# Kernel optimization log

Hardware: AMD Instinct MI355X
Metric: run time of the kernel (lower is better)

## Reference

```python
import jax, jax.numpy as jnp
import numpy as np

N_NODES = 100000
N_EDGES = 1600000
N_FEAT = 128
HIDDEN = 64
N_CLASSES = 40


def setup_inputs() -> dict:
    key = jax.random.key(0)
    ks = jax.random.split(key, 4)
    x = jax.random.normal(ks[0], (N_NODES, N_FEAT), dtype=jnp.float32)
    edge_index = jax.random.randint(ks[1], (2, N_EDGES), 0, N_NODES, dtype=jnp.int64)
    # Glorot-style init like PyG GCNConv
    W1 = jax.random.normal(ks[2], (N_FEAT, HIDDEN), dtype=jnp.float32) * (1.0 / np.sqrt(N_FEAT))
    b1 = jnp.zeros((HIDDEN,), dtype=jnp.float32)
    W2 = jax.random.normal(ks[3], (HIDDEN, N_CLASSES), dtype=jnp.float32) * (1.0 / np.sqrt(HIDDEN))
    b2 = jnp.zeros((N_CLASSES,), dtype=jnp.float32)
    return {"x": x, "edge_index": edge_index, "W1": W1, "b1": b1, "W2": W2, "b2": b2}


def _gcn_conv(x, src, dst, norm, W, b, n_nodes):
    # PyG GCNConv: transform first, then normalized scatter-add aggregation
    h = x @ W                                   # [N, out]
    msg = h[src] * norm[:, None]                # [E+N, out] gather
    out = jax.ops.segment_sum(msg, dst, num_segments=n_nodes)  # scatter-add
    return out + b


def _norm_and_loops(edge_index, n_nodes):
    # add self-loops, symmetric normalization deg^{-1/2} A_hat deg^{-1/2}
    loop = jnp.arange(n_nodes, dtype=edge_index.dtype)
    src = jnp.concatenate([edge_index[0], loop])
    dst = jnp.concatenate([edge_index[1], loop])
    deg = jax.ops.segment_sum(jnp.ones_like(dst, dtype=jnp.float32), dst, num_segments=n_nodes)
    dinv = jnp.where(deg > 0, jax.lax.rsqrt(jnp.maximum(deg, 1.0)), 0.0)
    norm = dinv[src] * dinv[dst]
    return src, dst, norm


def reference(x, edge_index, W1, b1, W2, b2):
    n_nodes = x.shape[0]
    src, dst, norm = _norm_and_loops(edge_index, n_nodes)
    h = _gcn_conv(x, src, dst, norm, W1, b1, n_nodes)
    h = jax.nn.relu(h)
    h = _gcn_conv(h, src, dst, norm, W2, b2, n_nodes)
    return jax.nn.log_softmax(h, axis=1)
```

## Files before the change

kernel.cpp:

```cpp
#include <hip/hip_runtime.h>
#include <hip/hip_bf16.h>
#include <string.h>

#define N_FEAT 128
#define HIDDEN 64
#define N_CLS  40
#define FILL_BLOCKS 2048
#define CHUNK_EDGES 16384
#define STAGE_CAP 4096
#define B_BITS 6
#define SRC_BITS 17

typedef __bf16 bf16x8 __attribute__((ext_vector_type(8)));
typedef float  f32x4  __attribute__((ext_vector_type(4)));

union Frag { unsigned u[4]; bf16x8 v; };

static __device__ inline int get_xcc() {
    return (int)(__builtin_amdgcn_s_getreg((3 << 11) | 20) & 7u);
}


static __device__ inline unsigned pack_bf16(float a, float b) {
    unsigned ba = __float_as_uint(a);
    unsigned bb = __float_as_uint(b);
    unsigned ra = (ba + 0x7fffu + ((ba >> 16) & 1u)) >> 16;
    unsigned rb = (bb + 0x7fffu + ((bb >> 16) & 1u)) >> 16;
    return (ra & 0xffffu) | (rb << 16);
}

static __device__ inline float2 unpack_bf16(unsigned v) {
    return make_float2(__uint_as_float(v << 16), __uint_as_float(v & 0xffff0000u));
}


__global__ void detect_layout_kernel(const int* __restrict__ ei, int* __restrict__ flag) {
    int lane = threadIdx.x;
    int v = ei[2 * lane + 1];
    unsigned long long b = __ballot(v != 0);
    if (lane == 0) flag[0] = (b == 0ull) ? 1 : 0;
}


__global__ __launch_bounds__(256) void bucket_hist_kernel(const int* __restrict__ ei,
                                                          const int* __restrict__ flag,
                                                          unsigned* __restrict__ bcnt8,
                                                          int E, int nbuk) {
    __shared__ unsigned h[2048];
    for (int i = threadIdx.x; i < nbuk; i += 256) h[i] = 0u;
    __syncthreads();
    bool is64 = (flag[0] != 0);
    if (is64) {
        int idx = blockIdx.x * 256 + threadIdx.x;
        int stride2 = gridDim.x * 256 * 2;
        int Eeven = E & ~1;
        for (int e = idx * 2; e < Eeven; e += stride2) {
            uint4 dv = *(const uint4*)(ei + (size_t)2 * E + (size_t)2 * e);
            atomicAdd(&h[((int)dv.x) >> B_BITS], 1u);
            atomicAdd(&h[((int)dv.z) >> B_BITS], 1u);
        }
        for (int e = Eeven + idx; e < E; e += gridDim.x * 256) {
            int d = ei[(size_t)2 * E + (size_t)2 * e];
            atomicAdd(&h[d >> B_BITS], 1u);
        }
    } else {
        const int* dstp = ei + E;
        for (int e = blockIdx.x * 256 + threadIdx.x; e < E; e += gridDim.x * 256) {
            int d = dstp[e];
            atomicAdd(&h[d >> B_BITS], 1u);
        }
    }
    __syncthreads();
    unsigned copy = (blockIdx.x & 7u) << 11;
    for (int i = threadIdx.x; i < nbuk; i += 256)
        if (h[i]) atomicAdd(&bcnt8[copy + i], h[i]);
}


__global__ __launch_bounds__(512) void bucket_scan_kernel(const unsigned* __restrict__ bcnt8,
                                                          unsigned* __restrict__ bbase,
                                                          unsigned* __restrict__ bcur, int nbuk) {
    __shared__ unsigned tmp[512];
    __shared__ unsigned carry;
    if (threadIdx.x == 0) carry = 0u;
    __syncthreads();
    for (int base = 0; base < nbuk; base += 512) {
        int i = base + threadIdx.x;
        unsigned v = 0u;
        if (i < nbuk) {
#pragma unroll
            for (int c = 0; c < 8; ++c) v += bcnt8[(c << 11) + i];
        }
        tmp[threadIdx.x] = v;
        __syncthreads();
#pragma unroll
        for (int off = 1; off < 512; off <<= 1) {
            unsigned t = (threadIdx.x >= (unsigned)off) ? tmp[threadIdx.x - off] : 0u;
            __syncthreads();
            tmp[threadIdx.x] += t;
            __syncthreads();
        }
        unsigned excl = tmp[threadIdx.x] - v + carry;
        if (i < nbuk) {
            bbase[i] = excl;
            bcur[(size_t)i * 16] = excl;
        }
        __syncthreads();
        if (threadIdx.x == 511) carry += tmp[511];
        __syncthreads();
    }
}


__global__ __launch_bounds__(256) void fill_buckets_kernel(const int* __restrict__ ei,
                                                           const int* __restrict__ flag,
                                                           unsigned* __restrict__ bcur,
                                                           unsigned* __restrict__ ctr,
                                                           unsigned* __restrict__ tmpbuf,
                                                           int E, int nbuk) {
    int r = get_xcc();
    int bpx = (nbuk + 7) >> 3;
    int blo = r * bpx;
    int bhi = min(nbuk, blo + bpx);
    int nlb = bhi - blo;
    bool is64 = (flag[0] != 0);
    const size_t dstoff = (size_t)2 * E;

    __shared__ unsigned stage[STAGE_CAP];
    __shared__ unsigned hist[256], lbase[256], lcur[256];
    __shared__ unsigned tail_s, chunk_s;

    int lane = threadIdx.x & 63;
    unsigned long long lmask_lt = (lane == 0) ? 0ull : ((~0ull) >> (64 - lane));

    auto stage_edge = [&](bool own, unsigned v, unsigned lb) {
        unsigned long long mask = __ballot(own ? 1 : 0);
        int cnt = __popcll(mask);
        if (cnt) {
            unsigned bp = 0;
            int leader = __builtin_ctzll(mask);
            if (lane == leader) bp = atomicAdd(&tail_s, (unsigned)cnt);
            bp = __shfl(bp, leader);
            if (own) {
                unsigned pos = bp + (unsigned)__popcll(mask & lmask_lt);
                if (pos < STAGE_CAP) {
                    stage[pos] = v;
                    atomicAdd(&hist[lb], 1u);
                } else {
                    unsigned slot = __hip_atomic_fetch_add(&bcur[(size_t)(blo + (int)lb) * 16], 1u,
                                                           __ATOMIC_RELAXED, __HIP_MEMORY_SCOPE_WORKGROUP);
                    tmpbuf[slot] = v & 0x7fffffu;
                }
            }
        }
    };

    for (;;) {
        if (threadIdx.x == 0) {
            chunk_s = __hip_atomic_fetch_add(&ctr[r * 64], 1u, __ATOMIC_RELAXED,
                                             __HIP_MEMORY_SCOPE_WORKGROUP);
            tail_s = 0u;
        }
        if (threadIdx.x < 256) { hist[threadIdx.x] = 0u; lcur[threadIdx.x] = 0u; }
        __syncthreads();
        long long base = (long long)chunk_s * CHUNK_EDGES;
        if (base >= E) break;
        int end = (int)min((long long)E, base + CHUNK_EDGES);

        if (is64) {
            for (int e = (int)base + 2 * threadIdx.x; e + 1 < end; e += 512) {
                uint4 sv = *(const uint4*)(ei + (size_t)2 * e);
                uint4 dv = *(const uint4*)(ei + dstoff + (size_t)2 * e);
                {
                    int d = (int)dv.x;
                    int b = d >> B_BITS;
                    bool own = (b >= blo && b < bhi);
                    unsigned lb = own ? (unsigned)(b - blo) : 0u;
                    unsigned v = (lb << 23) | ((unsigned)(d & ((1 << B_BITS) - 1)) << SRC_BITS) | sv.x;
                    stage_edge(own, v, lb);
                }
                {
                    int d = (int)dv.z;
                    int b = d >> B_BITS;
                    bool own = (b >= blo && b < bhi);
                    unsigned lb = own ? (unsigned)(b - blo) : 0u;
                    unsigned v = (lb << 23) | ((unsigned)(d & ((1 << B_BITS) - 1)) << SRC_BITS) | sv.z;
                    stage_edge(own, v, lb);
                }
            }
            if ((end - (int)base) & 1) {
                bool own = false; unsigned v = 0, lb = 0;
                if (threadIdx.x == 0) {
                    int e = end - 1;
                    int d = ei[dstoff + (size_t)2 * e];
                    int b = d >> B_BITS;
                    if (b >= blo && b < bhi) {
                        own = true; lb = (unsigned)(b - blo);
                        v = (lb << 23) | ((unsigned)(d & ((1 << B_BITS) - 1)) << SRC_BITS)
                            | (unsigned)ei[(size_t)2 * e];
                    }
                }
                stage_edge(own, v, lb);
            }
        } else {
            for (int e = (int)base + threadIdx.x; e < end; e += 256) {
                int d = ei[(size_t)E + e];
                int b = d >> B_BITS;
                bool own = (b >= blo && b < bhi);
                unsigned lb = own ? (unsigned)(b - blo) : 0u;
                unsigned v = (lb << 23) | ((unsigned)(d & ((1 << B_BITS) - 1)) << SRC_BITS)
                             | (own ? (unsigned)ei[e] : 0u);
                stage_edge(own, v, lb);
            }
        }
        __syncthreads();

        for (int lb = threadIdx.x; lb < nlb; lb += 256) {
            unsigned h = hist[lb];
            if (h) lbase[lb] = __hip_atomic_fetch_add(&bcur[(size_t)(blo + lb) * 16], h,
                                                      __ATOMIC_RELAXED, __HIP_MEMORY_SCOPE_WORKGROUP);
        }
        __syncthreads();

        unsigned tl = min(tail_s, (unsigned)STAGE_CAP);
        for (unsigned i = threadIdx.x; i < tl; i += 256) {
            unsigned v = stage[i];
            unsigned lb = v >> 23;
            unsigned off = atomicAdd(&lcur[lb], 1u);
            tmpbuf[lbase[lb] + off] = v & 0x7fffffu;
        }
        __syncthreads();
    }
}


__global__ __launch_bounds__(256) void bucket_to_csr_kernel(const unsigned* __restrict__ tmpbuf,
                                                            const unsigned* __restrict__ bbase,
                                                            unsigned* __restrict__ deg,
                                                            unsigned* __restrict__ rowptr,
                                                            float* __restrict__ dinv,
                                                            int* __restrict__ csr_src,
                                                            int nbuk, int N, int E) {
    int b = blockIdx.x;
    int tid = threadIdx.x;
    unsigned beg = bbase[b];
    unsigned end = (b + 1 < nbuk) ? bbase[b + 1] : (unsigned)E;
    int d0 = b << B_BITS;
    const int ND = 1 << B_BITS;
    __shared__ unsigned hist[ND], scn[ND], cur[ND];
    if (tid < ND) { hist[tid] = 0u; cur[tid] = 0u; }
    __syncthreads();
    for (unsigned i = beg + tid; i < end; i += 256)
        atomicAdd(&hist[tmpbuf[i] >> SRC_BITS], 1u);
    __syncthreads();
    if (tid == 0) {
        unsigned run = 0;
        for (int k = 0; k < ND; ++k) { scn[k] = run; run += hist[k]; }
    }
    __syncthreads();
    if (tid < ND) {
        int d = d0 + tid;
        if (d < N) {
            unsigned dg = hist[tid];
            deg[d] = dg;
            dinv[d] = rsqrtf((float)(dg + 1u));
            rowptr[d] = beg + scn[tid];
        }
    }
    __syncthreads();
    for (unsigned i = beg + tid; i < end; i += 256) {
        unsigned v = tmpbuf[i];
        unsigned dl = v >> SRC_BITS;
        unsigned s = v & ((1u << SRC_BITS) - 1u);
        unsigned p = atomicAdd(&cur[dl], 1u);
        csr_src[beg + scn[dl] + p] = (int)s;
    }
}


__global__ __launch_bounds__(256) void gemm1_mfma_kernel(const float* __restrict__ x,
                                                         const float* __restrict__ W1,
                                                         const float* __restrict__ dinv,
                                                         unsigned* __restrict__ h1b, int N) {
    int lane = threadIdx.x & 63;
    int quad = lane >> 4;
    int col  = lane & 15;

    Frag B[4][4];
#pragma unroll
    for (int c = 0; c < 4; ++c)
#pragma unroll
        for (int ks = 0; ks < 4; ++ks) {
            int n = c * 16 + col;
#pragma unroll
            for (int jj = 0; jj < 4; ++jj) {
                int k = ks * 32 + quad * 8 + 2 * jj;
                B[c][ks].u[jj] = pack_bf16(W1[k * HIDDEN + n], W1[(k + 1) * HIDDEN + n]);
            }
        }

    int wave_id = blockIdx.x * 4 + (threadIdx.x >> 6);
    int nwaves  = gridDim.x * 4;
    int ntiles  = (N + 15) >> 4;

    for (int rt = wave_id; rt < ntiles; rt += nwaves) {
        int rowA = rt * 16 + col;
        Frag A[4];
#pragma unroll
        for (int ks = 0; ks < 4; ++ks) {
            float4 a0 = make_float4(0.f, 0.f, 0.f, 0.f), a1 = a0;
            if (rowA < N) {
                const float4* ap = (const float4*)(x + (size_t)rowA * N_FEAT + ks * 32 + quad * 8);
                a0 = ap[0];
                a1 = ap[1];
            }
            A[ks].u[0] = pack_bf16(a0.x, a0.y);
            A[ks].u[1] = pack_bf16(a0.z, a0.w);
            A[ks].u[2] = pack_bf16(a1.x, a1.y);
            A[ks].u[3] = pack_bf16(a1.z, a1.w);
        }
        f32x4 acc[4] = {{0.f, 0.f, 0.f, 0.f}, {0.f, 0.f, 0.f, 0.f},
                        {0.f, 0.f, 0.f, 0.f}, {0.f, 0.f, 0.f, 0.f}};
#pragma unroll
        for (int ks = 0; ks < 4; ++ks)
#pragma unroll
            for (int c = 0; c < 4; ++c)
                acc[c] = __builtin_amdgcn_mfma_f32_16x16x32_bf16(A[ks].v, B[c][ks].v, acc[c], 0, 0, 0);

        int rowD = rt * 16 + quad * 4;
#pragma unroll
        for (int c = 0; c < 4; ++c)
#pragma unroll
            for (int r = 0; r < 4; ++r) {
                float v = acc[c][r];
                float nxt = __shfl_down(v, 1);
                int row = rowD + r;
                if (((lane & 1) == 0) && row < N) {
                    float dr = dinv[row];
                    h1b[(size_t)row * 32 + ((c * 16 + col) >> 1)] = pack_bf16(v * dr, nxt * dr);
                }
            }
    }
}


__global__ __launch_bounds__(256) void gemm2_mfma_kernel(const unsigned* __restrict__ actb,
                                                         const float* __restrict__ W2,
                                                         const float* __restrict__ dinv,
                                                         unsigned* __restrict__ h2a,
                                                         unsigned* __restrict__ h2c, int N) {
    int lane = threadIdx.x & 63;
    int quad = lane >> 4;
    int col  = lane & 15;

    Frag B[3][2];
#pragma unroll
    for (int c = 0; c < 3; ++c)
#pragma unroll
        for (int ks = 0; ks < 2; ++ks) {
            int n = c * 16 + col;
#pragma unroll
            for (int jj = 0; jj < 4; ++jj) {
                int k = ks * 32 + quad * 8 + 2 * jj;
                float w0 = (n < N_CLS) ? W2[k * N_CLS + n] : 0.f;
                float w1 = (n < N_CLS) ? W2[(k + 1) * N_CLS + n] : 0.f;
                B[c][ks].u[jj] = pack_bf16(w0, w1);
            }
        }

    int wave_id = blockIdx.x * 4 + (threadIdx.x >> 6);
    int nwaves  = gridDim.x * 4;
    int ntiles  = (N + 15) >> 4;

    for (int rt = wave_id; rt < ntiles; rt += nwaves) {
        int rowA = rt * 16 + col;
        Frag A[2];
#pragma unroll
        for (int ks = 0; ks < 2; ++ks) {
            uint4 u = make_uint4(0u, 0u, 0u, 0u);
            if (rowA < N)
                u = *(const uint4*)(actb + (size_t)rowA * 32 + ks * 16 + quad * 4);
            A[ks].u[0] = u.x; A[ks].u[1] = u.y; A[ks].u[2] = u.z; A[ks].u[3] = u.w;
        }
        f32x4 acc[3] = {{0.f, 0.f, 0.f, 0.f}, {0.f, 0.f, 0.f, 0.f}, {0.f, 0.f, 0.f, 0.f}};
#pragma unroll
        for (int ks = 0; ks < 2; ++ks)
#pragma unroll
            for (int c = 0; c < 3; ++c)
                acc[c] = __builtin_amdgcn_mfma_f32_16x16x32_bf16(A[ks].v, B[c][ks].v, acc[c], 0, 0, 0);

        int rowD = rt * 16 + quad * 4;
#pragma unroll
        for (int c = 0; c < 3; ++c)
#pragma unroll
            for (int r = 0; r < 4; ++r) {
                float v = acc[c][r];
                float nxt = __shfl_down(v, 1);
                int row = rowD + r;
                int pair = (c * 16 + col) >> 1;
                if (((lane & 1) == 0) && row < N) {
                    float dr = dinv[row];
                    if (pair < 16)
                        h2a[(size_t)row * 16 + pair] = pack_bf16(v * dr, nxt * dr);
                    else if (pair < 20)
                        h2c[(size_t)row * 4 + (pair - 16)] = pack_bf16(v * dr, nxt * dr);
                }
            }
    }
}


__global__ __launch_bounds__(256) void agg1_kernel(const unsigned* __restrict__ h1b,
                                                   const int* __restrict__ csr_src,
                                                   const unsigned* __restrict__ rowptr,
                                                   const unsigned* __restrict__ deg,
                                                   const float* __restrict__ dinv,
                                                   const float* __restrict__ b1,
                                                   unsigned* __restrict__ actb, int N) {
    int wave = threadIdx.x >> 6, lane = threadIdx.x & 63;
    int sub = lane >> 5, j = lane & 31;
    int d = blockIdx.x * 4 + wave;
    if (d >= N) return;
    float dv = dinv[d];
    float acc0 = 0.f, acc1 = 0.f;
    if (sub == 0) {
        float2 v = unpack_bf16(h1b[(size_t)d * 32 + j]);
        acc0 = v.x; acc1 = v.y;
    }
    unsigned beg = rowptr[d];
    int len = (int)deg[d];
    int i = 0;
    for (; i + 16 <= len; i += 16) {
        int s0 = csr_src[beg + i + sub];
        int s1 = csr_src[beg + i + 2 + sub];
        int s2 = csr_src[beg + i + 4 + sub];
        int s3 = csr_src[beg + i + 6 + sub];
        int s4 = csr_src[beg + i + 8 + sub];
        int s5 = csr_src[beg + i + 10 + sub];
        int s6 = csr_src[beg + i + 12 + sub];
        int s7 = csr_src[beg + i + 14 + sub];
        unsigned v0 = h1b[(size_t)s0 * 32 + j];
        unsigned v1 = h1b[(size_t)s1 * 32 + j];
        unsigned v2 = h1b[(size_t)s2 * 32 + j];
        unsigned v3 = h1b[(size_t)s3 * 32 + j];
        unsigned v4 = h1b[(size_t)s4 * 32 + j];
        unsigned v5 = h1b[(size_t)s5 * 32 + j];
        unsigned v6 = h1b[(size_t)s6 * 32 + j];
        unsigned v7 = h1b[(size_t)s7 * 32 + j];
        float2 a0 = unpack_bf16(v0), a1 = unpack_bf16(v1);
        float2 a2 = unpack_bf16(v2), a3 = unpack_bf16(v3);
        float2 a4 = unpack_bf16(v4), a5 = unpack_bf16(v5);
        float2 a6 = unpack_bf16(v6), a7 = unpack_bf16(v7);
        acc0 += a0.x + a1.x + a2.x + a3.x + a4.x + a5.x + a6.x + a7.x;
        acc1 += a0.y + a1.y + a2.y + a3.y + a4.y + a5.y + a6.y + a7.y;
    }
    for (; i + 8 <= len; i += 8) {
        int s0 = csr_src[beg + i + sub];
        int s1 = csr_src[beg + i + 2 + sub];
        int s2 = csr_src[beg + i + 4 + sub];
        int s3 = csr_src[beg + i + 6 + sub];
        unsigned v0 = h1b[(size_t)s0 * 32 + j];
        unsigned v1 = h1b[(size_t)s1 * 32 + j];
        unsigned v2 = h1b[(size_t)s2 * 32 + j];
        unsigned v3 = h1b[(size_t)s3 * 32 + j];
        float2 a0 = unpack_bf16(v0), a1 = unpack_bf16(v1);
        float2 a2 = unpack_bf16(v2), a3 = unpack_bf16(v3);
        acc0 += a0.x + a1.x + a2.x + a3.x;
        acc1 += a0.y + a1.y + a2.y + a3.y;
    }
    for (; i + 4 <= len; i += 4) {
        int sA = csr_src[beg + i + sub];
        int sB = csr_src[beg + i + 2 + sub];
        float2 a = unpack_bf16(h1b[(size_t)sA * 32 + j]);
        float2 b = unpack_bf16(h1b[(size_t)sB * 32 + j]);
        acc0 += a.x + b.x;
        acc1 += a.y + b.y;
    }
    for (; i < len; i += 2) {
        int e = i + sub;
        if (e < len) {
            int s = csr_src[beg + e];
            float2 a = unpack_bf16(h1b[(size_t)s * 32 + j]);
            acc0 += a.x;
            acc1 += a.y;
        }
    }
    acc0 += __shfl_xor(acc0, 32);
    acc1 += __shfl_xor(acc1, 32);
    if (sub == 0) {
        float2 bb = ((const float2*)b1)[j];
        float r0 = fmaxf(acc0 * dv + bb.x, 0.f);
        float r1 = fmaxf(acc1 * dv + bb.y, 0.f);
        actb[(size_t)d * 32 + j] = pack_bf16(r0, r1);
    }
}


__global__ __launch_bounds__(256) void agg2_lsm_kernel(const unsigned* __restrict__ h2a,
                                                       const unsigned* __restrict__ h2c,
                                                       const int* __restrict__ csr_src,
                                                       const unsigned* __restrict__ rowptr,
                                                       const unsigned* __restrict__ deg,
                                                       const float* __restrict__ dinv,
                                                       const float* __restrict__ b2,
                                                       float* __restrict__ out, int N) {
    int wave = threadIdx.x >> 6, lane = threadIdx.x & 63;
    int sub = lane >> 5, j = lane & 31;
    bool act = (j < 20);
    const unsigned* tab;
    unsigned str;
    if (j < 16) { tab = h2a + j; str = 16u; }
    else        { tab = h2c + (j - 16); str = 4u; }
    int d = blockIdx.x * 4 + wave;
    if (d >= N) return;
    float dv = dinv[d];
    float acc0 = 0.f, acc1 = 0.f;
    if (sub == 0 && act) {
        float2 v = unpack_bf16(tab[(size_t)d * str]);
        acc0 = v.x; acc1 = v.y;
    }
    unsigned beg = rowptr[d];
    int len = (int)deg[d];
    int i = 0;
    for (; i + 16 <= len; i += 16) {
        int s0 = csr_src[beg + i + sub];
        int s1 = csr_src[beg + i + 2 + sub];
        int s2 = csr_src[beg + i + 4 + sub];
        int s3 = csr_src[beg + i + 6 + sub];
        int s4 = csr_src[beg + i + 8 + sub];
        int s5 = csr_src[beg + i + 10 + sub];
        int s6 = csr_src[beg + i + 12 + sub];
        int s7 = csr_src[beg + i + 14 + sub];
        if (act) {
            float2 a0 = unpack_bf16(tab[(size_t)s0 * str]);
            float2 a1 = unpack_bf16(tab[(size_t)s1 * str]);
            float2 a2 = unpack_bf16(tab[(size_t)s2 * str]);
            float2 a3 = unpack_bf16(tab[(size_t)s3 * str]);
            float2 a4 = unpack_bf16(tab[(size_t)s4 * str]);
            float2 a5 = unpack_bf16(tab[(size_t)s5 * str]);
            float2 a6 = unpack_bf16(tab[(size_t)s6 * str]);
            float2 a7 = unpack_bf16(tab[(size_t)s7 * str]);
            acc0 += a0.x + a1.x + a2.x + a3.x + a4.x + a5.x + a6.x + a7.x;
            acc1 += a0.y + a1.y + a2.y + a3.y + a4.y + a5.y + a6.y + a7.y;
        }
    }
    for (; i + 8 <= len; i += 8) {
        int s0 = csr_src[beg + i + sub];
        int s1 = csr_src[beg + i + 2 + sub];
        int s2 = csr_src[beg + i + 4 + sub];
        int s3 = csr_src[beg + i + 6 + sub];
        if (act) {
            float2 a0 = unpack_bf16(tab[(size_t)s0 * str]);
            float2 a1 = unpack_bf16(tab[(size_t)s1 * str]);
            float2 a2 = unpack_bf16(tab[(size_t)s2 * str]);
            float2 a3 = unpack_bf16(tab[(size_t)s3 * str]);
            acc0 += a0.x + a1.x + a2.x + a3.x;
            acc1 += a0.y + a1.y + a2.y + a3.y;
        }
    }
    for (; i + 4 <= len; i += 4) {
        int sA = csr_src[beg + i + sub];
        int sB = csr_src[beg + i + 2 + sub];
        if (act) {
            float2 a = unpack_bf16(tab[(size_t)sA * str]);
            float2 b = unpack_bf16(tab[(size_t)sB * str]);
            acc0 += a.x + b.x;
            acc1 += a.y + b.y;
        }
    }
    for (; i < len; i += 2) {
        int e = i + sub;
        if (e < len && act) {
            int s = csr_src[beg + e];
            float2 a = unpack_bf16(tab[(size_t)s * str]);
            acc0 += a.x;
            acc1 += a.y;
        }
    }
    acc0 += __shfl_xor(acc0, 32);
    acc1 += __shfl_xor(acc1, 32);
    float v0 = -1e30f, v1 = -1e30f;
    if (act) {
        float2 bb = ((const float2*)b2)[j];
        v0 = acc0 * dv + bb.x;
        v1 = acc1 * dv + bb.y;
    }
    float m = fmaxf(v0, v1);
#pragma unroll
    for (int off = 32; off > 0; off >>= 1)
        m = fmaxf(m, __shfl_xor(m, off));
    float ex = (act && sub == 0) ? (expf(v0 - m) + expf(v1 - m)) : 0.f;
#pragma unroll
    for (int off = 32; off > 0; off >>= 1)
        ex += __shfl_xor(ex, off);
    float ls = logf(ex);
    if (act && sub == 0) {
        float2* orow = (float2*)(out + (size_t)d * N_CLS);
        orow[j] = make_float2(v0 - m - ls, v1 - m - ls);
    }
}


static inline size_t align_up(size_t x) { return (x + 255) & ~(size_t)255; }

extern "C" void kernel_launch(void* const* d_in, const int* in_sizes, int n_in,
                              void* d_out, int out_size, void* d_ws, size_t ws_size,
                              hipStream_t stream) {
    const float* x  = (const float*)d_in[0];
    const int*   ei = (const int*)d_in[1];
    const float* W1 = (const float*)d_in[2];
    const float* b1 = (const float*)d_in[3];
    const float* W2 = (const float*)d_in[4];
    const float* b2 = (const float*)d_in[5];

    int N = in_sizes[0] / N_FEAT;
    int E = in_sizes[1] / 2;
    int nbuk = (N + (1 << B_BITS) - 1) >> B_BITS;

    char* ws = (char*)d_ws;
    int*      flag    = (int*)ws;       ws += 256;
    unsigned* ctrs    = (unsigned*)ws;  ws += 4096;
    unsigned* bcnt8   = (unsigned*)ws;  ws += 8 * 2048 * 4;
    unsigned* bbase   = (unsigned*)ws;  ws += align_up((size_t)nbuk * 4);
    unsigned* bcur    = (unsigned*)ws;  ws += align_up((size_t)nbuk * 64);
    unsigned* deg     = (unsigned*)ws;  ws += align_up((size_t)N * 4);
    float*    dinv    = (float*)ws;     ws += align_up((size_t)N * 4);
    unsigned* rowptr  = (unsigned*)ws;  ws += align_up((size_t)N * 4);
    unsigned* tmpbuf  = (unsigned*)ws;  ws += align_up((size_t)E * 4);
    int*      csr_src = (int*)ws;       ws += align_up((size_t)E * 4);
    unsigned* h1b     = (unsigned*)ws;  ws += align_up((size_t)N * 32 * 4);
    unsigned* actb    = (unsigned*)ws;  ws += align_up((size_t)N * 32 * 4);
    unsigned* h2a     = (unsigned*)ws;  ws += align_up((size_t)N * 16 * 4);
    unsigned* h2c     = (unsigned*)ws;  ws += align_up((size_t)N * 4 * 4);

    hipMemsetAsync(ctrs, 0, 4096 + 8 * 2048 * 4, stream);

    detect_layout_kernel<<<1, 64, 0, stream>>>(ei, flag);
    bucket_hist_kernel<<<256, 256, 0, stream>>>(ei, flag, bcnt8, E, nbuk);
    bucket_scan_kernel<<<1, 512, 0, stream>>>(bcnt8, bbase, bcur, nbuk);
    fill_buckets_kernel<<<FILL_BLOCKS, 256, 0, stream>>>(ei, flag, bcur, ctrs, tmpbuf, E, nbuk);
    bucket_to_csr_kernel<<<nbuk, 256, 0, stream>>>(tmpbuf, bbase, deg, rowptr, dinv, csr_src, nbuk, N, E);

    gemm1_mfma_kernel<<<512, 256, 0, stream>>>(x, W1, dinv, h1b, N);
    agg1_kernel<<<(N + 3) / 4, 256, 0, stream>>>(h1b, csr_src, rowptr, deg, dinv, b1, actb, N);

    gemm2_mfma_kernel<<<512, 256, 0, stream>>>(actb, W2, dinv, h2a, h2c, N);
    agg2_lsm_kernel<<<(N + 3) / 4, 256, 0, stream>>>(h2a, h2c, csr_src, rowptr, deg, dinv, b2, (float*)d_out, N);
}
```

Before: 321.9 us.

## Replace LDS staging in bucket fill with two-pass histogram-then-scatter over chunk

```diff
diff --git a/kernel.cpp b/kernel.cpp
--- a/kernel.cpp
+++ b/kernel.cpp
@@ -6,8 +6,7 @@
 #define HIDDEN 64
 #define N_CLS  40
 #define FILL_BLOCKS 2048
-#define CHUNK_EDGES 16384
-#define STAGE_CAP 4096
+#define CHUNK_EDGES 8192
 #define B_BITS 6
 #define SRC_BITS 17
 
@@ -126,41 +125,13 @@
     bool is64 = (flag[0] != 0);
     const size_t dstoff = (size_t)2 * E;
 
-    __shared__ unsigned stage[STAGE_CAP];
     __shared__ unsigned hist[256], lbase[256], lcur[256];
-    __shared__ unsigned tail_s, chunk_s;
-
-    int lane = threadIdx.x & 63;
-    unsigned long long lmask_lt = (lane == 0) ? 0ull : ((~0ull) >> (64 - lane));
-
-    auto stage_edge = [&](bool own, unsigned v, unsigned lb) {
-        unsigned long long mask = __ballot(own ? 1 : 0);
-        int cnt = __popcll(mask);
-        if (cnt) {
-            unsigned bp = 0;
-            int leader = __builtin_ctzll(mask);
-            if (lane == leader) bp = atomicAdd(&tail_s, (unsigned)cnt);
-            bp = __shfl(bp, leader);
-            if (own) {
-                unsigned pos = bp + (unsigned)__popcll(mask & lmask_lt);
-                if (pos < STAGE_CAP) {
-                    stage[pos] = v;
-                    atomicAdd(&hist[lb], 1u);
-                } else {
-                    unsigned slot = __hip_atomic_fetch_add(&bcur[(size_t)(blo + (int)lb) * 16], 1u,
-                                                           __ATOMIC_RELAXED, __HIP_MEMORY_SCOPE_WORKGROUP);
-                    tmpbuf[slot] = v & 0x7fffffu;
-                }
-            }
-        }
-    };
+    __shared__ unsigned chunk_s;
 
     for (;;) {
-        if (threadIdx.x == 0) {
+        if (threadIdx.x == 0)
             chunk_s = __hip_atomic_fetch_add(&ctr[r * 64], 1u, __ATOMIC_RELAXED,
                                              __HIP_MEMORY_SCOPE_WORKGROUP);
-            tail_s = 0u;
-        }
         if (threadIdx.x < 256) { hist[threadIdx.x] = 0u; lcur[threadIdx.x] = 0u; }
         __syncthreads();
         long long base = (long long)chunk_s * CHUNK_EDGES;
@@ -169,65 +140,85 @@
 
         if (is64) {
             for (int e = (int)base + 2 * threadIdx.x; e + 1 < end; e += 512) {
-                uint4 sv = *(const uint4*)(ei + (size_t)2 * e);
+                uint4 dv = *(const uint4*)(ei + dstoff + (size_t)2 * e);
+                int b0 = ((int)dv.x) >> B_BITS;
+                int b1 = ((int)dv.z) >> B_BITS;
+                if (b0 >= blo && b0 < bhi) atomicAdd(&hist[b0 - blo], 1u);
+                if (b1 >= blo && b1 < bhi) atomicAdd(&hist[b1 - blo], 1u);
+            }
+            if ((end - (int)base) & 1) {
+                if (threadIdx.x == 0) {
+                    int d = ei[dstoff + (size_t)2 * (end - 1)];
+                    int b = d >> B_BITS;
+                    if (b >= blo && b < bhi) atomicAdd(&hist[b - blo], 1u);
+                }
+            }
+        } else {
+            for (int e = (int)base + threadIdx.x; e < end; e += 256) {
+                int b = ei[(size_t)E + e] >> B_BITS;
+                if (b >= blo && b < bhi) atomicAdd(&hist[b - blo], 1u);
+            }
+        }
+        __syncthreads();
+
+        for (int lb = threadIdx.x; lb < nlb; lb += 256) {
+            unsigned h = hist[lb];
+            if (h) lbase[lb] = __hip_atomic_fetch_add(&bcur[(size_t)(blo + lb) * 16], h,
+                                                      __ATOMIC_RELAXED, __HIP_MEMORY_SCOPE_WORKGROUP);
+        }
+        __syncthreads();
+
+        if (is64) {
+            for (int e = (int)base + 2 * threadIdx.x; e + 1 < end; e += 512) {
                 uint4 dv = *(const uint4*)(ei + dstoff + (size_t)2 * e);
                 {
                     int d = (int)dv.x;
                     int b = d >> B_BITS;
-                    bool own = (b >= blo && b < bhi);
-                    unsigned lb = own ? (unsigned)(b - blo) : 0u;
-                    unsigned v = (lb << 23) | ((unsigned)(d & ((1 << B_BITS) - 1)) << SRC_BITS) | sv.x;
-                    stage_edge(own, v, lb);
+                    if (b >= blo && b < bhi) {
+                        unsigned s = (unsigned)ei[(size_t)2 * e];
+                        int lb = b - blo;
+                        unsigned off = atomicAdd(&lcur[lb], 1u);
+                        tmpbuf[lbase[lb] + off] =
+                            ((unsigned)(d & ((1 << B_BITS) - 1)) << SRC_BITS) | s;
+                    }
                 }
                 {
                     int d = (int)dv.z;
                     int b = d >> B_BITS;
-                    bool own = (b >= blo && b < bhi);
-                    unsigned lb = own ? (unsigned)(b - blo) : 0u;
-                    unsigned v = (lb << 23) | ((unsigned)(d & ((1 << B_BITS) - 1)) << SRC_BITS) | sv.z;
-                    stage_edge(own, v, lb);
+                    if (b >= blo && b < bhi) {
+                        unsigned s = (unsigned)ei[(size_t)2 * (e + 1)];
+                        int lb = b - blo;
+                        unsigned off = atomicAdd(&lcur[lb], 1u);
+                        tmpbuf[lbase[lb] + off] =
+                            ((unsigned)(d & ((1 << B_BITS) - 1)) << SRC_BITS) | s;
+                    }
                 }
             }
             if ((end - (int)base) & 1) {
-                bool own = false; unsigned v = 0, lb = 0;
                 if (threadIdx.x == 0) {
                     int e = end - 1;
                     int d = ei[dstoff + (size_t)2 * e];
                     int b = d >> B_BITS;
                     if (b >= blo && b < bhi) {
-                        own = true; lb = (unsigned)(b - blo);
-                        v = (lb << 23) | ((unsigned)(d & ((1 << B_BITS) - 1)) << SRC_BITS)
+                        int lb = b - blo;
+                        unsigned off = atomicAdd(&lcur[lb], 1u);
+                        tmpbuf[lbase[lb] + off] =
+                            ((unsigned)(d & ((1 << B_BITS) - 1)) << SRC_BITS)
                             | (unsigned)ei[(size_t)2 * e];
                     }
                 }
-                stage_edge(own, v, lb);
             }
         } else {
             for (int e = (int)base + threadIdx.x; e < end; e += 256) {
                 int d = ei[(size_t)E + e];
                 int b = d >> B_BITS;
-                bool own = (b >= blo && b < bhi);
-                unsigned lb = own ? (unsigned)(b - blo) : 0u;
-                unsigned v = (lb << 23) | ((unsigned)(d & ((1 << B_BITS) - 1)) << SRC_BITS)
-                             | (own ? (unsigned)ei[e] : 0u);
-                stage_edge(own, v, lb);
-            }
-        }
-        __syncthreads();
-
-        for (int lb = threadIdx.x; lb < nlb; lb += 256) {
-            unsigned h = hist[lb];
-            if (h) lbase[lb] = __hip_atomic_fetch_add(&bcur[(size_t)(blo + lb) * 16], h,
-                                                      __ATOMIC_RELAXED, __HIP_MEMORY_SCOPE_WORKGROUP);
-        }
-        __syncthreads();
-
-        unsigned tl = min(tail_s, (unsigned)STAGE_CAP);
-        for (unsigned i = threadIdx.x; i < tl; i += 256) {
-            unsigned v = stage[i];
-            unsigned lb = v >> 23;
-            unsigned off = atomicAdd(&lcur[lb], 1u);
-            tmpbuf[lbase[lb] + off] = v & 0x7fffffu;
+                if (b >= blo && b < bhi) {
+                    int lb = b - blo;
+                    unsigned off = atomicAdd(&lcur[lb], 1u);
+                    tmpbuf[lbase[lb] + off] =
+                        ((unsigned)(d & ((1 << B_BITS) - 1)) << SRC_BITS) | (unsigned)ei[e];
+                }
+            }
         }
         __syncthreads();
     }
```

Measured after the change: 321.9 us. No clear change (-0.0%).
